# Optimization experiments

Hardware: AMD Instinct MI355X
Metric: run time of the kernel (lower is better)

The kernel has to match this reference:

```python
import jax, jax.numpy as jnp
import numpy as np

B, T, D = 8, 2048, 1024
E, S = 8, 1            # num_experts, num_slots
FF = 4 * (S * D)       # ffn_mult * (num_slots * hiddens)

def setup_inputs() -> dict:
    key = jax.random.key(0)
    ks = jax.random.split(key, 7)
    sd = S * D
    inp = {
        "X":  jax.random.normal(ks[0], (B, T, D), dtype=jnp.float32),
        # slots gating MLP (single linear D -> E*S)
        "Wg": jax.random.normal(ks[1], (D, E * S), dtype=jnp.float32) / np.sqrt(D),
        "bg": jnp.zeros((E * S,), dtype=jnp.float32),
        # expert FFN (weights SHARED across experts, as in source [FFN(...)]*E)
        "W1": jax.random.normal(ks[2], (sd, FF), dtype=jnp.float32) / np.sqrt(sd),
        "b1": jnp.zeros((FF,), dtype=jnp.float32),
        "W2": jax.random.normal(ks[3], (FF, sd), dtype=jnp.float32) / np.sqrt(FF),
        "b2": jnp.zeros((sd,), dtype=jnp.float32),
    }
    return inp

def reference(X, Wg, bg, W1, b1, W2, b2):
    # logits: (B, T, E*S)
    logits = jnp.einsum('btd,de->bte', X, Wg) + bg
    dispatch_w = jax.nn.softmax(logits, axis=1)   # over tokens T
    combine_w = jax.nn.softmax(logits, axis=2)    # over slots E*S
    # slots = dispatch_w^T @ X : (B, E*S, D) -> (B, E, S*D)
    slots = jnp.einsum('bte,btd->bed', dispatch_w, X).reshape(B, E, S * D)
    # shared-weight FFN applied per expert slot (dropout=0 at eval)
    h = jax.nn.silu(jnp.einsum('bef,fh->beh', slots, W1) + b1)
    y = jnp.einsum('beh,hf->bef', h, W2) + b2     # (B, E, S*D)
    y = y.reshape(B, E * S, D)
    # combine: (B, T, E*S) @ (B, E*S, D)
    return jnp.einsum('bte,bed->btd', combine_w, y)
```

## Files before the change

### kernel.cpp

```cpp
#include <hip/hip_runtime.h>
#include <math.h>

#define B_  8
#define T_  2048
#define D_  1024
#define E_  8
#define FF_ 4096
#define N_  64
#define BT_ (B_*T_)

#define LPART_F  0u
#define SPART_F  1048576u
#define G1PART_F 5242880u
#define G2PART_F 5767168u

__global__ __launch_bounds__(256) void k_logits_part(
    const float* __restrict__ X, const float* __restrict__ Wg,
    float* __restrict__ part)
{
    __shared__ float xt[256 * 36];

    const int tid = threadIdx.x;
    const int bt0 = blockIdx.x * 256;
    const int d0  = blockIdx.y * 128;

    float acc[8];
    #pragma unroll
    for (int e = 0; e < 8; ++e) acc[e] = 0.f;

    for (int dt = 0; dt < 4; ++dt) {
        if (dt) __syncthreads();
        #pragma unroll
        for (int r = 0; r < 8; ++r) {
            int fi = r * 256 + tid;
            int token = fi >> 3, dj = fi & 7;
            const float4 v = *(const float4*)
                &X[(size_t)(bt0 + token) * D_ + d0 + dt * 32 + dj * 4];
            *(float4*)&xt[token * 36 + dj * 4] = v;
        }
        __syncthreads();
        #pragma unroll
        for (int dj = 0; dj < 8; ++dj) {
            const float4 x4 = *(const float4*)&xt[tid * 36 + dj * 4];
            const int db = d0 + dt * 32 + dj * 4;
            const float xv[4] = {x4.x, x4.y, x4.z, x4.w};
            #pragma unroll
            for (int r = 0; r < 4; ++r) {
                const float4 wlo = *(const float4*)&Wg[(size_t)(db + r) * 8];
                const float4 whi = *(const float4*)&Wg[(size_t)(db + r) * 8 + 4];
                acc[0] += xv[r] * wlo.x; acc[1] += xv[r] * wlo.y;
                acc[2] += xv[r] * wlo.z; acc[3] += xv[r] * wlo.w;
                acc[4] += xv[r] * whi.x; acc[5] += xv[r] * whi.y;
                acc[6] += xv[r] * whi.z; acc[7] += xv[r] * whi.w;
            }
        }
    }

    float* pp = &part[LPART_F + (size_t)blockIdx.y * BT_ * E_
                      + (size_t)(bt0 + tid) * E_];
    *(float4*)&pp[0] = make_float4(acc[0], acc[1], acc[2], acc[3]);
    *(float4*)&pp[4] = make_float4(acc[4], acc[5], acc[6], acc[7]);
}

__global__ __launch_bounds__(256) void k_logits_merge(
    const float* __restrict__ part, const float* __restrict__ bg,
    float* __restrict__ logits, float* __restrict__ sexp_part)
{
    __shared__ float red[8 * 256];
    const int tid = threadIdx.x;
    const int token = blockIdx.x * 256 + tid;

    float a[8];
    #pragma unroll
    for (int e = 0; e < 8; ++e) a[e] = 0.f;
    #pragma unroll
    for (int p = 0; p < 8; ++p) {
        const float* pp = &part[LPART_F + (size_t)p * BT_ * E_
                                + (size_t)token * E_];
        const float4 v0 = *(const float4*)&pp[0];
        const float4 v1 = *(const float4*)&pp[4];
        a[0] += v0.x; a[1] += v0.y; a[2] += v0.z; a[3] += v0.w;
        a[4] += v1.x; a[5] += v1.y; a[6] += v1.z; a[7] += v1.w;
    }
    #pragma unroll
    for (int e = 0; e < 8; ++e) a[e] += bg[e];

    float* lp = &logits[(size_t)token * E_];
    *(float4*)&lp[0] = make_float4(a[0], a[1], a[2], a[3]);
    *(float4*)&lp[4] = make_float4(a[4], a[5], a[6], a[7]);

    #pragma unroll
    for (int e = 0; e < 8; ++e) red[e * 256 + tid] = expf(a[e]);
    __syncthreads();
    for (int s = 128; s >= 1; s >>= 1) {
        if (tid < s) {
            #pragma unroll
            for (int e = 0; e < 8; ++e)
                red[e * 256 + tid] += red[e * 256 + tid + s];
        }
        __syncthreads();
    }
    if (tid < 8) sexp_part[blockIdx.x * 8 + tid] = red[tid * 256];
}

__global__ __launch_bounds__(256) void k_slots_part(
    const float* __restrict__ X, const float* __restrict__ logits,
    const float* __restrict__ sexp_part, float* __restrict__ part)
{
    __shared__ float wlds[32 * 8];
    __shared__ float red[64];
    __shared__ float inv[8];

    const int tid = threadIdx.x;
    const int ts = blockIdx.x, b = blockIdx.y;
    const int t0 = ts * 32;

    if (tid < 64) red[tid] = sexp_part[b * 64 + tid];
    __syncthreads();
    if (tid < 8) {
        float s = 0.f;
        #pragma unroll
        for (int i = 0; i < 8; ++i) s += red[i * 8 + tid];
        inv[tid] = 1.f / s;
    }
    __syncthreads();
    {
        int t = tid >> 3, e = tid & 7;
        wlds[tid] = expf(logits[((size_t)b * T_ + t0 + t) * E_ + e]) * inv[e];
    }
    __syncthreads();

    float4 acc[8];
    #pragma unroll
    for (int e = 0; e < 8; ++e) acc[e] = make_float4(0.f, 0.f, 0.f, 0.f);

    const float* xb = &X[((size_t)b * T_ + t0) * D_ + tid * 4];
    #pragma unroll 8
    for (int t = 0; t < 32; ++t) {
        const float4 x4 = *(const float4*)&xb[(size_t)t * D_];
        const float4 wA = *(const float4*)&wlds[t * 8];
        const float4 wB = *(const float4*)&wlds[t * 8 + 4];
        const float w[8] = {wA.x, wA.y, wA.z, wA.w, wB.x, wB.y, wB.z, wB.w};
        #pragma unroll
        for (int e = 0; e < 8; ++e) {
            acc[e].x += x4.x * w[e];
            acc[e].y += x4.y * w[e];
            acc[e].z += x4.z * w[e];
            acc[e].w += x4.w * w[e];
        }
    }
    #pragma unroll
    for (int e = 0; e < 8; ++e) {
        *(float4*)&part[SPART_F + (size_t)ts * (N_ * D_)
                        + (size_t)(b * E_ + e) * D_ + tid * 4] = acc[e];
    }
}

__global__ __launch_bounds__(256) void k_reduce_slots(
    const float* __restrict__ part, float* __restrict__ slots)
{
    const int i = blockIdx.x * 256 + threadIdx.x;
    float s = 0.f;
    #pragma unroll
    for (int p = 0; p < 64; ++p)
        s += part[SPART_F + (size_t)p * (N_ * D_) + i];
    slots[i] = s;
}

template<int K, int F, int KSPLIT>
__global__ __launch_bounds__(256, 2) void k_ffn(
    const float* __restrict__ A, const float* __restrict__ W,
    float* __restrict__ part)
{
    __shared__ float As[64 * 132];

    const int tid = threadIdx.x;
    const int row = tid >> 2;
    const int cg  = tid & 3;
    const int f0  = blockIdx.x * 16 + cg * 4;
    const int k0  = blockIdx.y * (K / KSPLIT);

    float4 acc = make_float4(0.f, 0.f, 0.f, 0.f);

    for (int c = 0; c < (K / KSPLIT) / 128; ++c) {
        const int kb = k0 + c * 128;
        if (c) __syncthreads();
        #pragma unroll
        for (int i = 0; i < 8; ++i) {
            int idx = i * 256 + tid;
            int r = idx >> 5, kq = idx & 31;
            *(float4*)&As[r * 132 + kq * 4] =
                *(const float4*)&A[(size_t)r * K + kb + kq * 4];
        }
        __syncthreads();
        #pragma unroll 4
        for (int kq = 0; kq < 32; ++kq) {
            const float* wr = &W[(size_t)(kb + kq * 4) * F + f0];
            const float4 w0 = *(const float4*)&wr[0];
            const float4 w1 = *(const float4*)&wr[(size_t)F];
            const float4 w2 = *(const float4*)&wr[2 * (size_t)F];
            const float4 w3 = *(const float4*)&wr[3 * (size_t)F];
            const float4 a = *(const float4*)&As[row * 132 + kq * 4];
            acc.x += a.x*w0.x + a.y*w1.x + a.z*w2.x + a.w*w3.x;
            acc.y += a.x*w0.y + a.y*w1.y + a.z*w2.y + a.w*w3.y;
            acc.z += a.x*w0.z + a.y*w1.z + a.z*w2.z + a.w*w3.z;
            acc.w += a.x*w0.w + a.y*w1.w + a.z*w2.w + a.w*w3.w;
        }
    }

    *(float4*)&part[(size_t)blockIdx.y * (N_ * F) + (size_t)row * F + f0] = acc;
}

__global__ __launch_bounds__(256) void k_reduce_silu(
    const float* __restrict__ part, const float* __restrict__ b1,
    float* __restrict__ h)
{
    const int i4 = blockIdx.x * 256 + threadIdx.x;
    const float4 v0 = *(const float4*)&part[G1PART_F + (size_t)i4 * 4];
    const float4 v1 = *(const float4*)&part[G1PART_F + (size_t)(N_ * FF_) + (size_t)i4 * 4];
    const float4 bb = *(const float4*)&b1[(i4 & (FF_ / 4 - 1)) * 4];
    float4 r;
    r.x = v0.x + v1.x + bb.x; r.y = v0.y + v1.y + bb.y;
    r.z = v0.z + v1.z + bb.z; r.w = v0.w + v1.w + bb.w;
    r.x = r.x / (1.f + expf(-r.x));
    r.y = r.y / (1.f + expf(-r.y));
    r.z = r.z / (1.f + expf(-r.z));
    r.w = r.w / (1.f + expf(-r.w));
    *(float4*)&h[(size_t)i4 * 4] = r;
}

__global__ __launch_bounds__(256) void k_reduce_bias(
    const float* __restrict__ part, const float* __restrict__ b2,
    float* __restrict__ y)
{
    const int i4 = blockIdx.x * 256 + threadIdx.x;
    const float4 bb = *(const float4*)&b2[(i4 & (D_ / 4 - 1)) * 4];
    float4 r = bb;
    #pragma unroll
    for (int p = 0; p < 8; ++p) {
        const float4 v = *(const float4*)
            &part[G2PART_F + (size_t)p * (N_ * D_) + (size_t)i4 * 4];
        r.x += v.x; r.y += v.y; r.z += v.z; r.w += v.w;
    }
    *(float4*)&y[(size_t)i4 * 4] = r;
}

__global__ __launch_bounds__(256) void k_combine(
    const float* __restrict__ logits, const float* __restrict__ y,
    float* __restrict__ out)
{
    __shared__ float wlds[64 * 8];
    const int tid = threadIdx.x;
    const int dc = blockIdx.x, tc = blockIdx.y, b = blockIdx.z;
    const int t0 = tc * 64;

    if (tid < 64) {
        const float* lp = &logits[((size_t)b * T_ + t0 + tid) * E_];
        float ex[8]; float s = 0.f;
        #pragma unroll
        for (int i = 0; i < 8; ++i) { ex[i] = expf(lp[i]); s += ex[i]; }
        const float invs = 1.f / s;
        #pragma unroll
        for (int i = 0; i < 8; ++i) wlds[tid * 8 + i] = ex[i] * invs;
    }
    __syncthreads();

    const int d = dc * 256 + tid;
    float yv[8];
    #pragma unroll
    for (int e = 0; e < 8; ++e) yv[e] = y[(size_t)(b * E_ + e) * D_ + d];

    for (int t = 0; t < 64; ++t) {
        const float4 wA = *(const float4*)&wlds[t * 8];
        const float4 wB = *(const float4*)&wlds[t * 8 + 4];
        const float acc = wA.x*yv[0] + wA.y*yv[1] + wA.z*yv[2] + wA.w*yv[3]
                        + wB.x*yv[4] + wB.y*yv[5] + wB.z*yv[6] + wB.w*yv[7];
        out[((size_t)b * T_ + t0 + t) * D_ + d] = acc;
    }
}

extern "C" void kernel_launch(void* const* d_in, const int* in_sizes, int n_in,
                              void* d_out, int out_size, void* d_ws, size_t ws_size,
                              hipStream_t stream)
{
    const float* X  = (const float*)d_in[0];
    const float* Wg = (const float*)d_in[1];
    const float* bg = (const float*)d_in[2];
    const float* W1 = (const float*)d_in[3];
    const float* b1 = (const float*)d_in[4];
    const float* W2 = (const float*)d_in[5];
    const float* b2 = (const float*)d_in[6];
    float* out = (float*)d_out;

    float* wsf       = (float*)d_ws;
    float* logits    = wsf;
    float* sexp_part = logits + BT_ * E_;
    float* slots     = sexp_part + 512;
    float* h         = slots + N_ * D_;
    float* y         = h + N_ * FF_;

    hipLaunchKernelGGL(k_logits_part,  dim3(BT_ / 256, 8), dim3(256), 0, stream,
                       X, Wg, out);
    hipLaunchKernelGGL(k_logits_merge, dim3(BT_ / 256),    dim3(256), 0, stream,
                       out, bg, logits, sexp_part);
    hipLaunchKernelGGL(k_slots_part,   dim3(64, 8),        dim3(256), 0, stream,
                       X, logits, sexp_part, out);
    hipLaunchKernelGGL(k_reduce_slots, dim3(256),          dim3(256), 0, stream,
                       out, slots);
    hipLaunchKernelGGL((k_ffn<1024, 4096, 2>), dim3(FF_ / 16, 2), dim3(256), 0,
                       stream, slots, W1, out + G1PART_F);
    hipLaunchKernelGGL(k_reduce_silu,  dim3(256), dim3(256), 0, stream,
                       out, b1, h);
    hipLaunchKernelGGL((k_ffn<4096, 1024, 8>), dim3(D_ / 16, 8), dim3(256), 0,
                       stream, h, W2, out + G2PART_F);
    hipLaunchKernelGGL(k_reduce_bias,  dim3(64), dim3(256), 0, stream,
                       out, b2, y);
    hipLaunchKernelGGL(k_combine,      dim3(4, 32, 8), dim3(256), 0, stream,
                       logits, y, out);
}
```

Baseline: 284.3 us.

## Retile FFN GEMMs to 4x4 register blocks with fine K-split

The two FFN GEMM kernels now give each thread a 4-row by 4-column output tile, so each weight float4 load is reused across four activation rows instead of one. The K dimension is split into 64-wide chunks, which gives many more blocks (16 and 64 K-splits) and allows higher occupancy via launch bounds of 4. The reduction kernels are rewritten as scalar loops over 16 and 64 partial buffers, and the partial-buffer offset is moved to fit the larger scratch area. This cuts redundant weight traffic from L2 but increases partial-sum write and read traffic.

Result: faster. 274.4 us (-3.5%).

```diff
diff --git a/kernel.cpp b/kernel.cpp
--- a/kernel.cpp
+++ b/kernel.cpp
@@ -12,7 +12,7 @@
 #define LPART_F  0u
 #define SPART_F  1048576u
 #define G1PART_F 5242880u
-#define G2PART_F 5767168u
+#define G2PART_F 9437184u
 
 __global__ __launch_bounds__(256) void k_logits_part(
     const float* __restrict__ X, const float* __restrict__ Wg,
@@ -167,82 +167,77 @@
     slots[i] = s;
 }
 
-template<int K, int F, int KSPLIT>
-__global__ __launch_bounds__(256, 2) void k_ffn(
+template<int K, int F>
+__global__ __launch_bounds__(256, 4) void k_ffn(
     const float* __restrict__ A, const float* __restrict__ W,
     float* __restrict__ part)
 {
-    __shared__ float As[64 * 132];
-
-    const int tid = threadIdx.x;
-    const int row = tid >> 2;
-    const int cg  = tid & 3;
-    const int f0  = blockIdx.x * 16 + cg * 4;
-    const int k0  = blockIdx.y * (K / KSPLIT);
-
-    float4 acc = make_float4(0.f, 0.f, 0.f, 0.f);
-
-    for (int c = 0; c < (K / KSPLIT) / 128; ++c) {
-        const int kb = k0 + c * 128;
-        if (c) __syncthreads();
-        #pragma unroll
-        for (int i = 0; i < 8; ++i) {
-            int idx = i * 256 + tid;
-            int r = idx >> 5, kq = idx & 31;
-            *(float4*)&As[r * 132 + kq * 4] =
-                *(const float4*)&A[(size_t)r * K + kb + kq * 4];
-        }
-        __syncthreads();
-        #pragma unroll 4
-        for (int kq = 0; kq < 32; ++kq) {
-            const float* wr = &W[(size_t)(kb + kq * 4) * F + f0];
-            const float4 w0 = *(const float4*)&wr[0];
-            const float4 w1 = *(const float4*)&wr[(size_t)F];
-            const float4 w2 = *(const float4*)&wr[2 * (size_t)F];
-            const float4 w3 = *(const float4*)&wr[3 * (size_t)F];
-            const float4 a = *(const float4*)&As[row * 132 + kq * 4];
-            acc.x += a.x*w0.x + a.y*w1.x + a.z*w2.x + a.w*w3.x;
-            acc.y += a.x*w0.y + a.y*w1.y + a.z*w2.y + a.w*w3.y;
-            acc.z += a.x*w0.z + a.y*w1.z + a.z*w2.z + a.w*w3.z;
-            acc.w += a.x*w0.w + a.y*w1.w + a.z*w2.w + a.w*w3.w;
-        }
-    }
-
-    *(float4*)&part[(size_t)blockIdx.y * (N_ * F) + (size_t)row * F + f0] = acc;
+    __shared__ float As[64 * 68];
+
+    const int tid = threadIdx.x;
+    const int rg = tid >> 4;
+    const int cg = tid & 15;
+    const int f0 = blockIdx.x * 64 + cg * 4;
+    const int k0 = blockIdx.y * 64;
+
+    #pragma unroll
+    for (int i = 0; i < 4; ++i) {
+        int idx = i * 256 + tid;
+        int row = idx >> 4, kq = idx & 15;
+        *(float4*)&As[row * 68 + kq * 4] =
+            *(const float4*)&A[(size_t)row * K + k0 + kq * 4];
+    }
+    __syncthreads();
+
+    float4 acc[4];
+    #pragma unroll
+    for (int r = 0; r < 4; ++r) acc[r] = make_float4(0.f, 0.f, 0.f, 0.f);
+
+    #pragma unroll 4
+    for (int kq = 0; kq < 16; ++kq) {
+        const float* wr = &W[(size_t)(k0 + kq * 4) * F + f0];
+        const float4 w0 = *(const float4*)&wr[0];
+        const float4 w1 = *(const float4*)&wr[(size_t)F];
+        const float4 w2 = *(const float4*)&wr[2 * (size_t)F];
+        const float4 w3 = *(const float4*)&wr[3 * (size_t)F];
+        #pragma unroll
+        for (int r = 0; r < 4; ++r) {
+            const float4 a = *(const float4*)&As[(rg * 4 + r) * 68 + kq * 4];
+            acc[r].x += a.x*w0.x + a.y*w1.x + a.z*w2.x + a.w*w3.x;
+            acc[r].y += a.x*w0.y + a.y*w1.y + a.z*w2.y + a.w*w3.y;
+            acc[r].z += a.x*w0.z + a.y*w1.z + a.z*w2.z + a.w*w3.z;
+            acc[r].w += a.x*w0.w + a.y*w1.w + a.z*w2.w + a.w*w3.w;
+        }
+    }
+
+    float* pb = &part[(size_t)blockIdx.y * (N_ * F)];
+    #pragma unroll
+    for (int r = 0; r < 4; ++r)
+        *(float4*)&pb[(size_t)(rg * 4 + r) * F + f0] = acc[r];
 }
 
 __global__ __launch_bounds__(256) void k_reduce_silu(
     const float* __restrict__ part, const float* __restrict__ b1,
     float* __restrict__ h)
 {
-    const int i4 = blockIdx.x * 256 + threadIdx.x;
-    const float4 v0 = *(const float4*)&part[G1PART_F + (size_t)i4 * 4];
-    const float4 v1 = *(const float4*)&part[G1PART_F + (size_t)(N_ * FF_) + (size_t)i4 * 4];
-    const float4 bb = *(const float4*)&b1[(i4 & (FF_ / 4 - 1)) * 4];
-    float4 r;
-    r.x = v0.x + v1.x + bb.x; r.y = v0.y + v1.y + bb.y;
-    r.z = v0.z + v1.z + bb.z; r.w = v0.w + v1.w + bb.w;
-    r.x = r.x / (1.f + expf(-r.x));
-    r.y = r.y / (1.f + expf(-r.y));
-    r.z = r.z / (1.f + expf(-r.z));
-    r.w = r.w / (1.f + expf(-r.w));
-    *(float4*)&h[(size_t)i4 * 4] = r;
+    const int i = blockIdx.x * 256 + threadIdx.x;
+    float s = b1[i & (FF_ - 1)];
+    #pragma unroll
+    for (int p = 0; p < 16; ++p)
+        s += part[G1PART_F + (size_t)p * (N_ * FF_) + i];
+    h[i] = s / (1.f + expf(-s));
 }
 
 __global__ __launch_bounds__(256) void k_reduce_bias(
     const float* __restrict__ part, const float* __restrict__ b2,
     float* __restrict__ y)
 {
-    const int i4 = blockIdx.x * 256 + threadIdx.x;
-    const float4 bb = *(const float4*)&b2[(i4 & (D_ / 4 - 1)) * 4];
-    float4 r = bb;
-    #pragma unroll
-    for (int p = 0; p < 8; ++p) {
-        const float4 v = *(const float4*)
-            &part[G2PART_F + (size_t)p * (N_ * D_) + (size_t)i4 * 4];
-        r.x += v.x; r.y += v.y; r.z += v.z; r.w += v.w;
-    }
-    *(float4*)&y[(size_t)i4 * 4] = r;
+    const int i = blockIdx.x * 256 + threadIdx.x;
+    float s = b2[i & (D_ - 1)];
+    #pragma unroll
+    for (int p = 0; p < 64; ++p)
+        s += part[G2PART_F + (size_t)p * (N_ * D_) + i];
+    y[i] = s;
 }
 
 __global__ __launch_bounds__(256) void k_combine(
@@ -307,13 +302,13 @@
                        X, logits, sexp_part, out);
     hipLaunchKernelGGL(k_reduce_slots, dim3(256),          dim3(256), 0, stream,
                        out, slots);
-    hipLaunchKernelGGL((k_ffn<1024, 4096, 2>), dim3(FF_ / 16, 2), dim3(256), 0,
-                       stream, slots, W1, out + G1PART_F);
-    hipLaunchKernelGGL(k_reduce_silu,  dim3(256), dim3(256), 0, stream,
+    hipLaunchKernelGGL((k_ffn<1024, 4096>), dim3(FF_ / 64, 1024 / 64),
+                       dim3(256), 0, stream, slots, W1, out + G1PART_F);
+    hipLaunchKernelGGL(k_reduce_silu,  dim3(N_ * FF_ / 256), dim3(256), 0, stream,
                        out, b1, h);
-    hipLaunchKernelGGL((k_ffn<4096, 1024, 8>), dim3(D_ / 16, 8), dim3(256), 0,
-                       stream, h, W2, out + G2PART_F);
-    hipLaunchKernelGGL(k_reduce_bias,  dim3(64), dim3(256), 0, stream,
+    hipLaunchKernelGGL((k_ffn<4096, 1024>), dim3(D_ / 64, FF_ / 64),
+                       dim3(256), 0, stream, h, W2, out + G2PART_F);
+    hipLaunchKernelGGL(k_reduce_bias,  dim3(N_ * D_ / 256), dim3(256), 0, stream,
                        out, b2, y);
     hipLaunchKernelGGL(k_combine,      dim3(4, 32, 8), dim3(256), 0, stream,
                        logits, y, out);
```
